# Performance work log

Hardware: AMD Instinct MI355X
Metric: run time of the kernel (lower is better)

## Reference

```python
import jax, jax.numpy as jnp
import numpy as np
from jax import lax

PADDING = 1  # from init_kwargs; must equal (k-1)//2 so the residual add is shape-valid


def _conv_single(x, w):
    # x: [C_in, H, W], w: [C_out, C_in, kH, kW] -> [C_out, H, W]
    y = lax.conv_general_dilated(
        x[None],  # [1, C_in, H, W]
        w,
        window_strides=(1, 1),
        padding=[(PADDING, PADDING), (PADDING, PADDING)],
        dimension_numbers=("NCHW", "OIHW", "NCHW"),
    )
    return y[0]


def setup_inputs() -> dict:
    key = jax.random.key(0)
    k1, k2 = jax.random.split(key)
    B, C, H, W, K = 16, 128, 64, 64, 3
    inp = jax.random.normal(k1, (B, C, H, W), dtype=jnp.float32)
    # per-sample dynamic weights, scaled so conv output is O(1)
    weight = jax.random.normal(k2, (B, C, C, K, K), dtype=jnp.float32) * (1.0 / np.sqrt(C * K * K))
    return {"input": inp, "weight": weight}


def reference(input, weight):
    # per-sample conv2d with a different kernel per batch element + residual add
    residual = jax.vmap(_conv_single)(input, weight)  # [B, C, H, W]
    return input + residual
```

## Files before the change

### kernel.cpp

```cpp
#include <hip/hip_runtime.h>
#include <hip/hip_bf16.h>


typedef _Float16 h8 __attribute__((ext_vector_type(8)));
typedef _Float16 h4 __attribute__((ext_vector_type(4)));
typedef float f32x16 __attribute__((ext_vector_type(16)));
typedef float f4 __attribute__((ext_vector_type(4)));

#define MFMA32 __builtin_amdgcn_mfma_f32_32x32x16_f16

__device__ __forceinline__ void lds_load16(const void* g, void* l) {
#if __has_builtin(__builtin_amdgcn_global_load_lds)
    __builtin_amdgcn_global_load_lds((__attribute__((address_space(1))) const void*)g,
                                     (__attribute__((address_space(3))) void*)l, 16, 0, 0);
#else
    *(f4*)l = *(const f4*)g;
#endif
}

__global__ __launch_bounds__(256) void w_prepass(const float* __restrict__ W,
                                                 _Float16* __restrict__ wp) {
    __shared__ float raw[8 * 1153];
    const int bid = blockIdx.x;
    const int b   = bid >> 4;
    const int co0 = (bid & 15) * 8;
    const int t   = threadIdx.x;

    const float* src = W + (size_t)(b * 128 + co0) * 1152;
#pragma unroll
    for (int i = 0; i < 9; ++i) {
        int idx  = (i * 256 + t) * 4;
        f4 v     = *(const f4*)(src + idx);
        int co_l = idx / 1152;
        int rem  = idx - co_l * 1152;
        *(f4*)&raw[co_l * 1153 + rem] = v;
    }
    __syncthreads();

#pragma unroll
    for (int i = 0; i < 9; ++i) {
        int c    = i * 256 + t;
        int jh   = c & 1;
        int co_l = (c >> 1) & 7;
        int oct  = (c >> 4) & 3;
        int r    = c >> 6;
        int kw   = r % 3;
        int r2   = r / 3;
        int kc   = r2 & 3;
        int kh   = r2 >> 2;
        int cib  = kc * 32 + oct * 8 + jh * 4;
        h4 v;
#pragma unroll
        for (int jj = 0; jj < 4; ++jj)
            v[jj] = (_Float16)raw[co_l * 1153 + (cib + jj) * 9 + kh * 3 + kw];
        size_t o = ((size_t)(b * 3 + kh) * 4 + kc) * 12288 +
                   (size_t)(kw * 4 + oct) * 1024 + (size_t)(co0 + co_l) * 8 + jh * 4;
        *(h4*)&wp[o] = v;
    }
}


__global__ __launch_bounds__(256, 2) void conv_main(const float* __restrict__ X,
                                                    const _Float16* __restrict__ wp,
                                                    float* __restrict__ out) {
    __shared__ _Float16 sX[2 * 4224];
    __shared__ _Float16 sW[2 * 12288];

    const int t    = threadIdx.x;
    const int lane = t & 63;
    const int l31  = lane & 31;
    const int lhi  = lane >> 5;
    const int wv   = t >> 6;
    const int wvM  = wv >> 1;
    const int wr   = wv & 1;

    const int bid   = blockIdx.x;
    const int swz   = (bid & 7) * 64 + (bid >> 3);
    const int batch = swz >> 5;
    const int h0    = (swz & 31) * 2;

    const int sy  = t >> 7;
    const int xq  = (t & 15) * 4;
    const int cio = (t >> 4) & 7;

    f32x16 acc[2][2];
#pragma unroll
    for (int mt = 0; mt < 2; ++mt)
#pragma unroll
        for (int nt = 0; nt < 2; ++nt)
#pragma unroll
            for (int r = 0; r < 16; ++r) acc[mt][nt][r] = 0.f;

    if (t < 32) {
        int pb = t >> 4, y = (t >> 3) & 1, oct = (t >> 1) & 3, side = t & 1;
        h8 z = {};
        *(h8*)&sX[pb * 4224 + ((y * 4 + oct) * 66 + side * 65) * 8] = z;
    }

    f4 xrv[4];

    auto issue_stage = [&](int s, int pb) {
        const int kh = s >> 2, kc = s & 3;
        const _Float16* wsrc = wp + ((size_t)(batch * 3 + kh) * 4 + kc) * 12288 + (size_t)t * 8;
        _Float16* wdst = sW + pb * 12288 + t * 8;
#pragma unroll
        for (int r = 0; r < 6; ++r)
            lds_load16(wsrc + (size_t)r * 2048, wdst + r * 2048);
        const int yy = h0 + sy + kh - 1;
        if (yy >= 0 && yy < 64) {
            const float* xp = X + ((size_t)(batch * 128 + kc * 32 + cio * 4) * 64 + yy) * 64 + xq;
#pragma unroll
            for (int j = 0; j < 4; ++j) xrv[j] = *(const f4*)(xp + (size_t)j * 4096);
        } else {
#pragma unroll
            for (int j = 0; j < 4; ++j) xrv[j] = (f4){0.f, 0.f, 0.f, 0.f};
        }
    };

    auto write_x = [&](int pb) {
#pragma unroll
        for (int k = 0; k < 4; ++k) {
            h4 v = {(_Float16)xrv[0][k], (_Float16)xrv[1][k],
                    (_Float16)xrv[2][k], (_Float16)xrv[3][k]};
            *(h4*)&sX[pb * 4224 + ((sy * 4 + (cio >> 1)) * 66 + xq + 1 + k) * 8 + (cio & 1) * 4] = v;
        }
    };

    auto compute = [&](int pb) {
        const _Float16* sWp = sW + pb * 12288;
        const _Float16* sXp = sX + pb * 4224;
#pragma unroll
        for (int ks = 0; ks < 6; ++ks) {
            const int kw = ks >> 1, kk = ks & 1;
            h8 af[2], bf[2];
#pragma unroll
            for (int mt = 0; mt < 2; ++mt)
                af[mt] = *(const h8*)&sWp[((kw * 4 + kk * 2 + lhi) * 128 + wvM * 64 + mt * 32 + l31) * 8];
#pragma unroll
            for (int nt = 0; nt < 2; ++nt)
                bf[nt] = *(const h8*)&sXp[((wr * 4 + kk * 2 + lhi) * 66 + nt * 32 + l31 + kw) * 8];
#pragma unroll
            for (int mt = 0; mt < 2; ++mt)
#pragma unroll
                for (int nt = 0; nt < 2; ++nt)
                    acc[mt][nt] = MFMA32(af[mt], bf[nt], acc[mt][nt], 0, 0, 0);
        }
    };

    issue_stage(0, 0);
    write_x(0);
    asm volatile("s_waitcnt vmcnt(0)" ::: "memory");
    __syncthreads();

    int p = 0;
#pragma unroll 1
    for (int s = 0; s < 11; ++s) {
        issue_stage(s + 1, p ^ 1);
        compute(p);
        write_x(p ^ 1);
        asm volatile("s_waitcnt vmcnt(0)" ::: "memory");
        __syncthreads();
        p ^= 1;
    }
    compute(p);

#pragma unroll
    for (int mt = 0; mt < 2; ++mt)
#pragma unroll
        for (int nt = 0; nt < 2; ++nt)
#pragma unroll
            for (int rg = 0; rg < 16; ++rg) {
                int co = wvM * 64 + mt * 32 + (rg & 3) + 8 * (rg >> 2) + 4 * lhi;
                int x  = nt * 32 + l31;
                size_t o = ((size_t)(batch * 128 + co) * 64 + h0 + wr) * 64 + x;
                out[o] = X[o] + acc[mt][nt][rg];
            }
}

extern "C" void kernel_launch(void* const* d_in, const int* in_sizes, int n_in,
                              void* d_out, int out_size, void* d_ws, size_t ws_size,
                              hipStream_t stream) {
    const float* inp = (const float*)d_in[0];
    const float* wgt = (const float*)d_in[1];
    float* out = (float*)d_out;
    _Float16* wpk = (_Float16*)d_ws;

    w_prepass<<<256, 256, 0, stream>>>(wgt, wpk);
    conv_main<<<512, 256, 0, stream>>>(inp, wpk, out);
}
```

Before: 111.8 us.

## Read packed weight fragments directly from global memory instead of staging in LDS

Removes the LDS double-buffer for weights: each wave now loads its MFMA A-fragments straight from the pre-packed fp16 weight buffer in global memory. Only the input tile stays staged in LDS. This drops the 48KB weight LDS footprint and the explicit vmcnt waits, which could allow higher occupancy. The cost is global/L2 latency on the critical path inside compute, since each wave fetches its own copy of fragments shared across waves. It also wraps the MFMA groups in s_setprio to favour matrix issue.

```diff
diff --git a/kernel.cpp b/kernel.cpp
--- a/kernel.cpp
+++ b/kernel.cpp
@@ -8,15 +8,6 @@
 typedef float f4 __attribute__((ext_vector_type(4)));
 
 #define MFMA32 __builtin_amdgcn_mfma_f32_32x32x16_f16
-
-__device__ __forceinline__ void lds_load16(const void* g, void* l) {
-#if __has_builtin(__builtin_amdgcn_global_load_lds)
-    __builtin_amdgcn_global_load_lds((__attribute__((address_space(1))) const void*)g,
-                                     (__attribute__((address_space(3))) void*)l, 16, 0, 0);
-#else
-    *(f4*)l = *(const f4*)g;
-#endif
-}
 
 __global__ __launch_bounds__(256) void w_prepass(const float* __restrict__ W,
                                                  _Float16* __restrict__ wp) {
@@ -64,7 +55,6 @@
                                                     const _Float16* __restrict__ wp,
                                                     float* __restrict__ out) {
     __shared__ _Float16 sX[2 * 4224];
-    __shared__ _Float16 sW[2 * 12288];
 
     const int t    = threadIdx.x;
     const int lane = t & 63;
@@ -99,13 +89,10 @@
 
     f4 xrv[4];
 
-    auto issue_stage = [&](int s, int pb) {
+    const int wrow = (lhi * 128 + wvM * 64 + l31) * 8;
+
+    auto load_x = [&](int s) {
         const int kh = s >> 2, kc = s & 3;
-        const _Float16* wsrc = wp + ((size_t)(batch * 3 + kh) * 4 + kc) * 12288 + (size_t)t * 8;
-        _Float16* wdst = sW + pb * 12288 + t * 8;
-#pragma unroll
-        for (int r = 0; r < 6; ++r)
-            lds_load16(wsrc + (size_t)r * 2048, wdst + r * 2048);
         const int yy = h0 + sy + kh - 1;
         if (yy >= 0 && yy < 64) {
             const float* xp = X + ((size_t)(batch * 128 + kc * 32 + cio * 4) * 64 + yy) * 64 + xq;
@@ -126,8 +113,9 @@
         }
     };
 
-    auto compute = [&](int pb) {
-        const _Float16* sWp = sW + pb * 12288;
+    auto compute = [&](int s, int pb) {
+        const int kh = s >> 2, kc = s & 3;
+        const _Float16* wbase = wp + ((size_t)(batch * 3 + kh) * 4 + kc) * 12288 + wrow;
         const _Float16* sXp = sX + pb * 4224;
 #pragma unroll
         for (int ks = 0; ks < 6; ++ks) {
@@ -135,34 +123,34 @@
             h8 af[2], bf[2];
 #pragma unroll
             for (int mt = 0; mt < 2; ++mt)
-                af[mt] = *(const h8*)&sWp[((kw * 4 + kk * 2 + lhi) * 128 + wvM * 64 + mt * 32 + l31) * 8];
+                af[mt] = *(const h8*)&wbase[(size_t)((kw * 4 + kk * 2) * 128 + mt * 32) * 8];
 #pragma unroll
             for (int nt = 0; nt < 2; ++nt)
                 bf[nt] = *(const h8*)&sXp[((wr * 4 + kk * 2 + lhi) * 66 + nt * 32 + l31 + kw) * 8];
+            __builtin_amdgcn_s_setprio(1);
 #pragma unroll
             for (int mt = 0; mt < 2; ++mt)
 #pragma unroll
                 for (int nt = 0; nt < 2; ++nt)
                     acc[mt][nt] = MFMA32(af[mt], bf[nt], acc[mt][nt], 0, 0, 0);
+            __builtin_amdgcn_s_setprio(0);
         }
     };
 
-    issue_stage(0, 0);
+    load_x(0);
     write_x(0);
-    asm volatile("s_waitcnt vmcnt(0)" ::: "memory");
     __syncthreads();
 
     int p = 0;
 #pragma unroll 1
     for (int s = 0; s < 11; ++s) {
-        issue_stage(s + 1, p ^ 1);
-        compute(p);
+        load_x(s + 1);
+        compute(s, p);
         write_x(p ^ 1);
-        asm volatile("s_waitcnt vmcnt(0)" ::: "memory");
         __syncthreads();
         p ^= 1;
     }
-    compute(p);
+    compute(11, p);
 
 #pragma unroll
     for (int mt = 0; mt < 2; ++mt)
```

Measured after the change: 120.6 us. 7.8% more time.
